# Optimization experiments

Hardware: AMD Instinct MI355X
Metric: run time of the kernel (lower is better)

## Reference

```python
import jax, jax.numpy as jnp
import numpy as np

EPS = 1e-8

def setup_inputs() -> dict:
    key = jax.random.key(0)
    k1, k2, k3, k4, k5 = jax.random.split(key, 5)
    B, S, d, H = 4, 1024, 512, 8
    hd = d // H
    x = jax.random.normal(k1, (B, S, d), dtype=jnp.float32)
    V = jax.random.normal(k2, (B, S, H, hd), dtype=jnp.float32)
    # binary biological mask [B, S, S]
    M = (jax.random.uniform(k3, (B, S, S)) > 0.5).astype(jnp.float32)
    in_proj_w = jax.random.normal(k4, (3 * d, d), dtype=jnp.float32) * 0.02
    in_proj_b = jnp.zeros((3 * d,), dtype=jnp.float32)
    out_w = jax.random.normal(k5, (d, d), dtype=jnp.float32) * 0.02
    out_b = jnp.zeros((d,), dtype=jnp.float32)
    return {"x": x, "V": V, "M": M, "in_proj_w": in_proj_w,
            "in_proj_b": in_proj_b, "out_w": out_w, "out_b": out_b}


def reference(x, V, M, in_proj_w, in_proj_b, out_w, out_b):
    B, S, d = x.shape
    H, hd = V.shape[2], V.shape[3]
    # packed QKV projection (torch MHA in_proj); V slice is computed by torch
    # but its result is discarded, so only Q,K slices influence the output.
    qkv = x @ in_proj_w.T + in_proj_b            # [B, S, 3d]
    q = qkv[..., :d].reshape(B, S, H, hd).transpose(0, 2, 1, 3)        # [B,H,S,hd]
    k = qkv[..., d:2 * d].reshape(B, S, H, hd).transpose(0, 2, 1, 3)   # [B,H,S,hd]
    scores = jnp.einsum("bhqd,bhkd->bhqk", q, k) / jnp.sqrt(jnp.float32(hd))
    A = jax.nn.softmax(scores, axis=-1)           # [B,H,S,S] per-head attn weights
    # biological mask + L1 renormalization (post-hoc, as in original)
    A_sparse = A * M[:, None, :, :]
    norm = jnp.sum(jnp.abs(A_sparse), axis=-1, keepdims=True) + EPS
    A_bar = A_sparse / norm
    # custom V: [B,S,H,hd] -> [B,H,S,hd]
    Vp = V.transpose(0, 2, 1, 3)
    out = jnp.einsum("bhqk,bhkd->bhqd", A_bar, Vp)  # [B,H,S,hd]
    out = out.transpose(0, 2, 1, 3).reshape(B, S, d)
    return out @ out_w.T + out_b
```

## Files before the change

kernel.cpp:

```cpp
#include <hip/hip_runtime.h>
#include <hip/hip_bf16.h>

#define BB 4
#define SS 1024
#define DD 512
#define HH 8
#define HD 64

typedef __attribute__((ext_vector_type(8))) short bf16x8;
typedef __attribute__((ext_vector_type(4))) float f32x4;

static __device__ __forceinline__ unsigned short f2b(float f) {
  union { float f; unsigned int u; } c; c.f = f;
  return (unsigned short)((c.u + 0x7fffu + ((c.u >> 16) & 1u)) >> 16);
}

__global__ __launch_bounds__(256) void prep(
    const float* __restrict__ x, const float* __restrict__ W1,
    const float* __restrict__ Wo, const float* __restrict__ Mmask,
    const float* __restrict__ V, unsigned short* __restrict__ xb,
    unsigned short* __restrict__ W1b, unsigned short* __restrict__ Wob,
    unsigned char* __restrict__ Mpack, unsigned short* __restrict__ Vt) {
  __shared__ float Ls[64][65];
  const int bid = blockIdx.x;
  const int tid = threadIdx.x;

  if (bid < 1408) {
    const float* src; unsigned short* dst; size_t off;
    if (bid < 1024) { src = x;  dst = xb;  off = ((size_t)bid * 256 + tid) * 8; }
    else if (bid < 1280) { src = W1; dst = W1b; off = ((size_t)(bid - 1024) * 256 + tid) * 8; }
    else { src = Wo; dst = Wob; off = ((size_t)(bid - 1280) * 256 + tid) * 8; }
    const float4 a = *(const float4*)(src + off);
    const float4 b = *(const float4*)(src + off + 4);
    union { unsigned short s[8]; uint4 v; } o;
    o.s[0] = f2b(a.x); o.s[1] = f2b(a.y); o.s[2] = f2b(a.z); o.s[3] = f2b(a.w);
    o.s[4] = f2b(b.x); o.s[5] = f2b(b.y); o.s[6] = f2b(b.z); o.s[7] = f2b(b.w);
    *(uint4*)(dst + off) = o.v;
  } else if (bid < 3456) {
    const size_t g = (size_t)(bid - 1408) * 256 + tid;
    const float4 a = *(const float4*)(Mmask + g * 8);
    const float4 b = *(const float4*)(Mmask + g * 8 + 4);
    unsigned v = 0;
    v |= (a.x > 0.5f) ? 1u : 0u;   v |= (a.y > 0.5f) ? 2u : 0u;
    v |= (a.z > 0.5f) ? 4u : 0u;   v |= (a.w > 0.5f) ? 8u : 0u;
    v |= (b.x > 0.5f) ? 16u : 0u;  v |= (b.y > 0.5f) ? 32u : 0u;
    v |= (b.z > 0.5f) ? 64u : 0u;  v |= (b.w > 0.5f) ? 128u : 0u;
    Mpack[g] = (unsigned char)v;
  } else {
    const int id = bid - 3456;
    const int s0 = (id & 15) * 64, h = (id >> 4) & 7, b = id >> 7;
    {
      const int r = tid >> 2, cs = (tid & 3) * 16;
      const float* src = V + ((size_t)((b * SS + s0 + r) * HH) + h) * HD + cs;
#pragma unroll
      for (int j = 0; j < 4; j++) {
        const float4 v = *(const float4*)(src + j * 4);
        Ls[r][cs + j * 4 + 0] = v.x; Ls[r][cs + j * 4 + 1] = v.y;
        Ls[r][cs + j * 4 + 2] = v.z; Ls[r][cs + j * 4 + 3] = v.w;
      }
    }
    __syncthreads();
    {
      const int d = tid >> 2, ss = (tid & 3) * 16;
      union { unsigned short s[16]; uint4 v[2]; } o;
#pragma unroll
      for (int j = 0; j < 16; j++) o.s[j] = f2b(Ls[ss + j][d]);
      unsigned short* dst =
          Vt + ((size_t)((b * HH + h) * HD + d)) * SS + s0 + ss;
      *(uint4*)dst = o.v[0];
      *(uint4*)(dst + 8) = o.v[1];
    }
  }
}

__global__ __launch_bounds__(256) void gemm_qk(
    const unsigned short* __restrict__ xb, const unsigned short* __restrict__ W1b,
    const float* __restrict__ bias, unsigned short* __restrict__ qkb) {
  __shared__ unsigned short As[128][40];
  __shared__ unsigned short Bs[64][40];
  const int tid = threadIdx.x;
  const int lane = tid & 63, wave = tid >> 6;
  const int l16 = lane & 15, quad = lane >> 4;
  const int row0 = blockIdx.y * 128, col0 = blockIdx.x * 64;

  f32x4 acc[2][4];
#pragma unroll
  for (int i = 0; i < 2; i++)
#pragma unroll
    for (int j = 0; j < 4; j++) acc[i][j] = (f32x4){0.f, 0.f, 0.f, 0.f};

  const int ra = tid >> 1, csa = (tid & 1) * 16;
  const int rb = tid >> 2, csb = (tid & 3) * 8;
  const unsigned short* ap = xb + (size_t)(row0 + ra) * DD + csa;
  const unsigned short* bp = W1b + (size_t)(col0 + rb) * DD + csb;

  uint4 pa0 = *(const uint4*)ap, pa1 = *(const uint4*)(ap + 8);
  uint4 pb = *(const uint4*)bp;

  for (int k0 = 0; k0 < DD; k0 += 32) {
    __syncthreads();
    *(uint4*)&As[ra][csa] = pa0;
    *(uint4*)&As[ra][csa + 8] = pa1;
    *(uint4*)&Bs[rb][csb] = pb;
    __syncthreads();
    if (k0 + 32 < DD) {
      pa0 = *(const uint4*)(ap + k0 + 32);
      pa1 = *(const uint4*)(ap + k0 + 40);
      pb = *(const uint4*)(bp + k0 + 32);
    }

    const bf16x8 a0 = *(const bf16x8*)&As[wave * 32 + l16][quad * 8];
    const bf16x8 a1 = *(const bf16x8*)&As[wave * 32 + 16 + l16][quad * 8];
#pragma unroll
    for (int nt = 0; nt < 4; nt++) {
      const bf16x8 bb = *(const bf16x8*)&Bs[nt * 16 + l16][quad * 8];
      acc[0][nt] = __builtin_amdgcn_mfma_f32_16x16x32_bf16(a0, bb, acc[0][nt], 0, 0, 0);
      acc[1][nt] = __builtin_amdgcn_mfma_f32_16x16x32_bf16(a1, bb, acc[1][nt], 0, 0, 0);
    }
  }

#pragma unroll
  for (int nt = 0; nt < 4; nt++) {
    const int col = col0 + nt * 16 + l16;
    const float bv = bias[col];
    const float scale = (col < DD) ? 0.125f : 1.0f;
#pragma unroll
    for (int mi = 0; mi < 2; mi++)
#pragma unroll
      for (int reg = 0; reg < 4; reg++) {
        const int row = row0 + wave * 32 + mi * 16 + quad * 4 + reg;
        qkb[(size_t)row * 1024 + col] = f2b((acc[mi][nt][reg] + bv) * scale);
      }
  }
}

__global__ __launch_bounds__(256) void gemm_out(
    const unsigned short* __restrict__ Ab, const unsigned short* __restrict__ Wob,
    const float* __restrict__ bias, float* __restrict__ out) {
  __shared__ unsigned short As[64][40];
  __shared__ unsigned short Bs[64][40];
  const int tid = threadIdx.x;
  const int lane = tid & 63, wave = tid >> 6;
  const int l16 = lane & 15, quad = lane >> 4;
  const int row0 = blockIdx.y * 64, col0 = blockIdx.x * 64;

  f32x4 acc[4];
#pragma unroll
  for (int j = 0; j < 4; j++) acc[j] = (f32x4){0.f, 0.f, 0.f, 0.f};

  const int r = tid >> 2, cs = (tid & 3) * 8;
  const unsigned short* ap = Ab + (size_t)(row0 + r) * DD + cs;
  const unsigned short* bp = Wob + (size_t)(col0 + r) * DD + cs;

  uint4 pa = *(const uint4*)ap;
  uint4 pb = *(const uint4*)bp;

  for (int k0 = 0; k0 < DD; k0 += 32) {
    __syncthreads();
    *(uint4*)&As[r][cs] = pa;
    *(uint4*)&Bs[r][cs] = pb;
    __syncthreads();
    if (k0 + 32 < DD) {
      pa = *(const uint4*)(ap + k0 + 32);
      pb = *(const uint4*)(bp + k0 + 32);
    }

    const bf16x8 a0 = *(const bf16x8*)&As[wave * 16 + l16][quad * 8];
#pragma unroll
    for (int nt = 0; nt < 4; nt++) {
      const bf16x8 bb = *(const bf16x8*)&Bs[nt * 16 + l16][quad * 8];
      acc[nt] = __builtin_amdgcn_mfma_f32_16x16x32_bf16(a0, bb, acc[nt], 0, 0, 0);
    }
  }

#pragma unroll
  for (int nt = 0; nt < 4; nt++) {
    const int col = col0 + nt * 16 + l16;
    const float bv = bias[col];
#pragma unroll
    for (int reg = 0; reg < 4; reg++) {
      const int row = row0 + wave * 16 + quad * 4 + reg;
      out[(size_t)row * DD + col] = acc[nt][reg] + bv;
    }
  }
}

__global__ __launch_bounds__(256) void flash_attn_split(
    const unsigned short* __restrict__ qkb, const unsigned short* __restrict__ Vt,
    const unsigned char* __restrict__ Mpack, float* __restrict__ Opart,
    float* __restrict__ Sms) {
  __shared__ unsigned short QP[64][72];
  __shared__ unsigned short Ks[64][72];
  __shared__ unsigned short Vs[64][72];

  const int tid = threadIdx.x;
  const int lane = tid & 63, wave = tid >> 6;
  const int l16 = lane & 15, quad = lane >> 4;
  const int q0 = blockIdx.x * 64;
  const int h = blockIdx.y & 7, sp = blockIdx.y >> 3;
  const int b = blockIdx.z;

  const int r = tid >> 2, cs = (tid & 3) * 16;

  {
    const unsigned short* s = qkb + (size_t)(b * SS + q0 + r) * 1024 + h * HD + cs;
    *(uint4*)&QP[r][cs] = *(const uint4*)s;
    *(uint4*)&QP[r][cs + 8] = *(const uint4*)(s + 8);
  }

  union { uint4 v[4]; unsigned w[16]; } mu;
  {
    const uint4* mp = (const uint4*)(Mpack +
        (size_t)(b * SS + q0 + wave * 16 + l16) * 128 + sp * 64);
    mu.v[0] = mp[0]; mu.v[1] = mp[1]; mu.v[2] = mp[2]; mu.v[3] = mp[3];
  }

  __syncthreads();
  const bf16x8 bQ0 = *(const bf16x8*)&QP[wave * 16 + l16][quad * 8];
  const bf16x8 bQ1 = *(const bf16x8*)&QP[wave * 16 + l16][32 + quad * 8];
  unsigned short(*Ps)[72] = (unsigned short(*)[72]) & QP[wave * 16][0];

  float Smp = 0.f;
  f32x4 O[4];
#pragma unroll
  for (int i = 0; i < 4; i++) O[i] = (f32x4){0.f, 0.f, 0.f, 0.f};

  const unsigned short* kp =
      qkb + (size_t)(b * SS + sp * 8 * 64 + r) * 1024 + DD + h * HD + cs;
  const unsigned short* vp =
      Vt + ((size_t)((b * HH + h) * HD + r)) * SS + sp * 8 * 64 + cs;

  uint4 pk0 = *(const uint4*)kp, pk1 = *(const uint4*)(kp + 8);
  uint4 pv0 = *(const uint4*)vp, pv1 = *(const uint4*)(vp + 8);

#pragma unroll
  for (int i = 0; i < 8; i++) {
    const unsigned mlo = mu.w[2 * i], mhi = mu.w[2 * i + 1];

    __syncthreads();
    *(uint4*)&Ks[r][cs] = pk0;
    *(uint4*)&Ks[r][cs + 8] = pk1;
    *(uint4*)&Vs[r][cs] = pv0;
    *(uint4*)&Vs[r][cs + 8] = pv1;
    __syncthreads();

    if (i < 7) {
      const unsigned short* nk = kp + (size_t)(i + 1) * 64 * 1024;
      const unsigned short* nv = vp + (i + 1) * 64;
      pk0 = *(const uint4*)nk; pk1 = *(const uint4*)(nk + 8);
      pv0 = *(const uint4*)nv; pv1 = *(const uint4*)(nv + 8);
    }

#pragma unroll
    for (int t = 0; t < 4; t++) {
      const bf16x8 aK0 = *(const bf16x8*)&Ks[t * 16 + l16][quad * 8];
      const bf16x8 aK1 = *(const bf16x8*)&Ks[t * 16 + l16][32 + quad * 8];
      f32x4 a = (f32x4){0.f, 0.f, 0.f, 0.f};
      a = __builtin_amdgcn_mfma_f32_16x16x32_bf16(aK0, bQ0, a, 0, 0, 0);
      a = __builtin_amdgcn_mfma_f32_16x16x32_bf16(aK1, bQ1, a, 0, 0, 0);
      const unsigned nib =
          ((t < 2 ? mlo : mhi) >> ((t & 1) * 16 + quad * 4)) & 0xFu;
      float e0 = __expf(a[0]); e0 = (nib & 1u) ? e0 : 0.f;
      float e1 = __expf(a[1]); e1 = (nib & 2u) ? e1 : 0.f;
      float e2 = __expf(a[2]); e2 = (nib & 4u) ? e2 : 0.f;
      float e3 = __expf(a[3]); e3 = (nib & 8u) ? e3 : 0.f;
      Smp += (e0 + e1) + (e2 + e3);
      uint2 w;
      w.x = (unsigned)f2b(e0) | ((unsigned)f2b(e1) << 16);
      w.y = (unsigned)f2b(e2) | ((unsigned)f2b(e3) << 16);
      *(uint2*)&Ps[l16][t * 16 + quad * 4] = w;
    }

    const bf16x8 aP0 = *(const bf16x8*)&Ps[l16][quad * 8];
    const bf16x8 aP1 = *(const bf16x8*)&Ps[l16][32 + quad * 8];
#pragma unroll
    for (int dt = 0; dt < 4; dt++) {
      const bf16x8 bV0 = *(const bf16x8*)&Vs[dt * 16 + l16][quad * 8];
      const bf16x8 bV1 = *(const bf16x8*)&Vs[dt * 16 + l16][32 + quad * 8];
      O[dt] = __builtin_amdgcn_mfma_f32_16x16x32_bf16(aP0, bV0, O[dt], 0, 0, 0);
      O[dt] = __builtin_amdgcn_mfma_f32_16x16x32_bf16(aP1, bV1, O[dt], 0, 0, 0);
    }
  }

  Smp += __shfl_xor(Smp, 16);
  Smp += __shfl_xor(Smp, 32);
  const size_t grow0 = (size_t)(b * HH + h) * SS + q0 + wave * 16;
  const int NR = BB * HH * SS;
  if (lane < 16) Sms[(size_t)sp * NR + grow0 + lane] = Smp;
#pragma unroll
  for (int reg = 0; reg < 4; reg++) {
    const size_t obase = ((size_t)sp * NR + grow0 + quad * 4 + reg) * HD;
#pragma unroll
    for (int dt = 0; dt < 4; dt++)
      Opart[obase + dt * 16 + l16] = O[dt][reg];
  }
}

__global__ __launch_bounds__(256) void combine(
    const float* __restrict__ Opart, const float* __restrict__ Sms,
    unsigned short* __restrict__ attnb) {
  const int idx = blockIdx.x * 256 + threadIdx.x;
  const int row = idx >> 4;
  const int d = (idx & 15) * 4;
  const int NR = BB * HH * SS;
  const float4 o0 = *(const float4*)(Opart + (size_t)row * HD + d);
  const float4 o1 = *(const float4*)(Opart + ((size_t)NR + row) * HD + d);
  const float s = Sms[row] + Sms[NR + row];
  const float inv = 1.0f / (s + 1e-12f);
  const int b = row >> 13, h = (row >> 10) & 7, q = row & 1023;
  union { unsigned short us[4]; uint2 v; } o;
  o.us[0] = f2b((o0.x + o1.x) * inv);
  o.us[1] = f2b((o0.y + o1.y) * inv);
  o.us[2] = f2b((o0.z + o1.z) * inv);
  o.us[3] = f2b((o0.w + o1.w) * inv);
  *(uint2*)(attnb + (size_t)(b * SS + q) * DD + h * HD + d) = o.v;
}

extern "C" void kernel_launch(void* const* d_in, const int* in_sizes, int n_in,
                              void* d_out, int out_size, void* d_ws,
                              size_t ws_size, hipStream_t stream) {
  const float* x = (const float*)d_in[0];
  const float* V = (const float*)d_in[1];
  const float* Mmask = (const float*)d_in[2];
  const float* in_proj_w = (const float*)d_in[3];
  const float* in_proj_b = (const float*)d_in[4];
  const float* out_w = (const float*)d_in[5];
  const float* out_b = (const float*)d_in[6];
  float* out = (float*)d_out;

  unsigned char* ws = (unsigned char*)d_ws;
  unsigned short* qkb   = (unsigned short*)(ws);
  unsigned short* xb    = (unsigned short*)(ws + (8ull << 20));
  unsigned short* W1b   = (unsigned short*)(ws + (12ull << 20));
  unsigned short* Wob   = (unsigned short*)(ws + (13ull << 20));
  unsigned short* Vt    = (unsigned short*)(ws + (14ull << 20));
  unsigned short* attnb = (unsigned short*)(ws + (18ull << 20));
  float*          Opart = (float*)(ws + (22ull << 20));
  float*          Sms   = (float*)(ws + (38ull << 20));
  unsigned char*  Mpack = ws + (38ull << 20) + (256u << 10);

  prep<<<3968, 256, 0, stream>>>(x, in_proj_w, out_w, Mmask, V,
                                 xb, W1b, Wob, Mpack, Vt);
  gemm_qk<<<dim3(16, 32), 256, 0, stream>>>(xb, W1b, in_proj_b, qkb);
  flash_attn_split<<<dim3(SS / 64, 2 * HH, BB), 256, 0, stream>>>(
      qkb, Vt, Mpack, Opart, Sms);
  combine<<<2048, 256, 0, stream>>>(Opart, Sms, attnb);
  gemm_out<<<dim3(8, 64), 256, 0, stream>>>(attnb, Wob, out_b, out);
}
```

Before: 135.7 us.

## Drop key-split in flash attention and fuse combine normalization into epilogue

The attention kernel now walks all 16 key tiles in one block instead of splitting keys across two blocks. It normalizes by the row sum in its epilogue and writes bf16 output directly. This removes the separate combine kernel and the fp32 partial-output and row-sum buffers, along with their global round-trip. In exchange the grid is halved, which lowers parallelism. The mask bits are now loaded per tile inside the loop rather than up front.

```diff
diff --git a/kernel.cpp b/kernel.cpp
--- a/kernel.cpp
+++ b/kernel.cpp
@@ -185,19 +185,19 @@
   }
 }
 
-__global__ __launch_bounds__(256) void flash_attn_split(
+__global__ __launch_bounds__(256) void flash_attn(
     const unsigned short* __restrict__ qkb, const unsigned short* __restrict__ Vt,
-    const unsigned char* __restrict__ Mpack, float* __restrict__ Opart,
-    float* __restrict__ Sms) {
+    const unsigned char* __restrict__ Mpack, unsigned short* __restrict__ attnb) {
   __shared__ unsigned short QP[64][72];
   __shared__ unsigned short Ks[64][72];
   __shared__ unsigned short Vs[64][72];
+  __shared__ float SmT[4][16];
 
   const int tid = threadIdx.x;
   const int lane = tid & 63, wave = tid >> 6;
   const int l16 = lane & 15, quad = lane >> 4;
   const int q0 = blockIdx.x * 64;
-  const int h = blockIdx.y & 7, sp = blockIdx.y >> 3;
+  const int h = blockIdx.y;
   const int b = blockIdx.z;
 
   const int r = tid >> 2, cs = (tid & 3) * 16;
@@ -207,35 +207,29 @@
     *(uint4*)&QP[r][cs] = *(const uint4*)s;
     *(uint4*)&QP[r][cs + 8] = *(const uint4*)(s + 8);
   }
-
-  union { uint4 v[4]; unsigned w[16]; } mu;
-  {
-    const uint4* mp = (const uint4*)(Mpack +
-        (size_t)(b * SS + q0 + wave * 16 + l16) * 128 + sp * 64);
-    mu.v[0] = mp[0]; mu.v[1] = mp[1]; mu.v[2] = mp[2]; mu.v[3] = mp[3];
-  }
-
   __syncthreads();
   const bf16x8 bQ0 = *(const bf16x8*)&QP[wave * 16 + l16][quad * 8];
   const bf16x8 bQ1 = *(const bf16x8*)&QP[wave * 16 + l16][32 + quad * 8];
   unsigned short(*Ps)[72] = (unsigned short(*)[72]) & QP[wave * 16][0];
 
+  const unsigned char* mrowp =
+      Mpack + (size_t)(b * SS + q0 + wave * 16 + l16) * 128;
+
   float Smp = 0.f;
   f32x4 O[4];
 #pragma unroll
   for (int i = 0; i < 4; i++) O[i] = (f32x4){0.f, 0.f, 0.f, 0.f};
 
-  const unsigned short* kp =
-      qkb + (size_t)(b * SS + sp * 8 * 64 + r) * 1024 + DD + h * HD + cs;
-  const unsigned short* vp =
-      Vt + ((size_t)((b * HH + h) * HD + r)) * SS + sp * 8 * 64 + cs;
+  const unsigned short* kp = qkb + (size_t)(b * SS + r) * 1024 + DD + h * HD + cs;
+  const unsigned short* vp = Vt + ((size_t)((b * HH + h) * HD + r)) * SS + cs;
 
   uint4 pk0 = *(const uint4*)kp, pk1 = *(const uint4*)(kp + 8);
   uint4 pv0 = *(const uint4*)vp, pv1 = *(const uint4*)(vp + 8);
-
-#pragma unroll
-  for (int i = 0; i < 8; i++) {
-    const unsigned mlo = mu.w[2 * i], mhi = mu.w[2 * i + 1];
+  uint2 pm = *(const uint2*)mrowp;
+
+#pragma unroll 4
+  for (int i = 0; i < 16; i++) {
+    const unsigned mlo = pm.x, mhi = pm.y;
 
     __syncthreads();
     *(uint4*)&Ks[r][cs] = pk0;
@@ -244,11 +238,12 @@
     *(uint4*)&Vs[r][cs + 8] = pv1;
     __syncthreads();
 
-    if (i < 7) {
+    if (i < 15) {
       const unsigned short* nk = kp + (size_t)(i + 1) * 64 * 1024;
       const unsigned short* nv = vp + (i + 1) * 64;
       pk0 = *(const uint4*)nk; pk1 = *(const uint4*)(nk + 8);
       pv0 = *(const uint4*)nv; pv1 = *(const uint4*)(nv + 8);
+      pm = *(const uint2*)(mrowp + (i + 1) * 8);
     }
 
 #pragma unroll
@@ -284,36 +279,18 @@
 
   Smp += __shfl_xor(Smp, 16);
   Smp += __shfl_xor(Smp, 32);
-  const size_t grow0 = (size_t)(b * HH + h) * SS + q0 + wave * 16;
-  const int NR = BB * HH * SS;
-  if (lane < 16) Sms[(size_t)sp * NR + grow0 + lane] = Smp;
+  if (lane < 16) SmT[wave][lane] = Smp;
+  float invr[4];
+#pragma unroll
+  for (int reg = 0; reg < 4; reg++)
+    invr[reg] = 1.0f / (SmT[wave][quad * 4 + reg] + 1e-12f);
 #pragma unroll
   for (int reg = 0; reg < 4; reg++) {
-    const size_t obase = ((size_t)sp * NR + grow0 + quad * 4 + reg) * HD;
+    const size_t row = (size_t)(b * SS + q0 + wave * 16 + quad * 4 + reg);
 #pragma unroll
     for (int dt = 0; dt < 4; dt++)
-      Opart[obase + dt * 16 + l16] = O[dt][reg];
-  }
-}
-
-__global__ __launch_bounds__(256) void combine(
-    const float* __restrict__ Opart, const float* __restrict__ Sms,
-    unsigned short* __restrict__ attnb) {
-  const int idx = blockIdx.x * 256 + threadIdx.x;
-  const int row = idx >> 4;
-  const int d = (idx & 15) * 4;
-  const int NR = BB * HH * SS;
-  const float4 o0 = *(const float4*)(Opart + (size_t)row * HD + d);
-  const float4 o1 = *(const float4*)(Opart + ((size_t)NR + row) * HD + d);
-  const float s = Sms[row] + Sms[NR + row];
-  const float inv = 1.0f / (s + 1e-12f);
-  const int b = row >> 13, h = (row >> 10) & 7, q = row & 1023;
-  union { unsigned short us[4]; uint2 v; } o;
-  o.us[0] = f2b((o0.x + o1.x) * inv);
-  o.us[1] = f2b((o0.y + o1.y) * inv);
-  o.us[2] = f2b((o0.z + o1.z) * inv);
-  o.us[3] = f2b((o0.w + o1.w) * inv);
-  *(uint2*)(attnb + (size_t)(b * SS + q) * DD + h * HD + d) = o.v;
+      attnb[row * DD + h * HD + dt * 16 + l16] = f2b(O[dt][reg] * invr[reg]);
+  }
 }
 
 extern "C" void kernel_launch(void* const* d_in, const int* in_sizes, int n_in,
@@ -335,15 +312,11 @@
   unsigned short* Wob   = (unsigned short*)(ws + (13ull << 20));
   unsigned short* Vt    = (unsigned short*)(ws + (14ull << 20));
   unsigned short* attnb = (unsigned short*)(ws + (18ull << 20));
-  float*          Opart = (float*)(ws + (22ull << 20));
-  float*          Sms   = (float*)(ws + (38ull << 20));
-  unsigned char*  Mpack = ws + (38ull << 20) + (256u << 10);
+  unsigned char*  Mpack = ws + (22ull << 20);
 
   prep<<<3968, 256, 0, stream>>>(x, in_proj_w, out_w, Mmask, V,
                                  xb, W1b, Wob, Mpack, Vt);
   gemm_qk<<<dim3(16, 32), 256, 0, stream>>>(xb, W1b, in_proj_b, qkb);
-  flash_attn_split<<<dim3(SS / 64, 2 * HH, BB), 256, 0, stream>>>(
-      qkb, Vt, Mpack, Opart, Sms);
-  combine<<<2048, 256, 0, stream>>>(Opart, Sms, attnb);
+  flash_attn<<<dim3(SS / 64, HH, BB), 256, 0, stream>>>(qkb, Vt, Mpack, attnb);
   gemm_out<<<dim3(8, 64), 256, 0, stream>>>(attnb, Wob, out_b, out);
 }
```

Measured after the change: 137.0 us. No clear change (+0.9%).
